# Kernel tuning notes

Measured on AMD Instinct MI355X. Metric: run time of the kernel, lower is better.

The kernel has to match this reference:

```python
import jax, jax.numpy as jnp
import numpy as np

H = 2        # num_heads
C = 128      # in_channels
K_ORDER = 4
BETA = 0.5


def _gcn_conv(x, row, col, deg_inv, n):
    # x: [N, H, C]; adj_t = D^{-1} A^T where A[row, col] = 1
    # (adj_t @ x)[c] = deg_inv[c] * sum_{e: col_e == c} x[row_e]
    msg = x[row]  # [E, H, C]
    agg = jax.ops.segment_sum(msg, col, num_segments=n)  # [N, H, C]
    return agg * deg_inv[:, None, None]


def _attn_conv(qs, ks, vs):
    # linear (kernelized) attention, non-block path
    n = qs.shape[0]
    kvs = jnp.einsum('lhm,lhd->hmd', ks, vs)            # [H, C, C]
    qkvs = jnp.einsum('nhm,hmd->nhd', qs, kvs)          # [N, H, C]
    vs_sum = vs.sum(axis=0)                             # [H, C]
    num = qkvs + vs_sum[None, :, :]
    ks_sum = ks.sum(axis=0)                             # [H, C]
    qks_sum = jnp.einsum('nhm,hm->nh', qs, ks_sum)[:, :, None]  # [N, H, 1]
    den = qks_sum + jnp.asarray(n, qs.dtype)
    return num / den


def setup_inputs() -> dict:
    key = jax.random.key(0)
    ks = jax.random.split(key, 8)
    N, E = 100000, 1600000
    x = jax.random.normal(ks[0], (N, C), jnp.float32)
    edge_index = jax.random.randint(ks[1], (2, E), 0, N, jnp.int64)
    s_in = 1.0 / np.sqrt(C)
    s_out = 1.0 / np.sqrt(H * C * (K_ORDER + 1))
    Wq_w = jax.random.normal(ks[2], (C, H * C), jnp.float32) * s_in
    Wq_b = jax.random.normal(ks[3], (H * C,), jnp.float32) * s_in
    Wk_w = jax.random.normal(ks[4], (C, H * C), jnp.float32) * s_in
    Wk_b = jax.random.normal(ks[5], (H * C,), jnp.float32) * s_in
    Wo_w = jax.random.normal(ks[6], (H * C * (K_ORDER + 1), C), jnp.float32) * s_out
    Wo_b = jax.random.normal(ks[7], (C,), jnp.float32) * s_out
    return {"x": x, "edge_index": edge_index, "Wq_w": Wq_w, "Wq_b": Wq_b,
            "Wk_w": Wk_w, "Wk_b": Wk_b, "Wo_w": Wo_w, "Wo_b": Wo_b}


def reference(x, edge_index, Wq_w, Wq_b, Wk_w, Wk_b, Wo_w, Wo_b):
    n = x.shape[0]
    row, col = edge_index[0], edge_index[1]
    # normalized adjacency D^{-1} A^T (pow(-1.0) in the source, not -0.5)
    deg = jax.ops.segment_sum(jnp.ones(row.shape[0], x.dtype), col, num_segments=n)
    deg_inv = jnp.where(deg > 0, 1.0 / deg, 0.0)

    query = (x @ Wq_w + Wq_b).reshape(n, H, C)
    key = (x @ Wk_w + Wk_b).reshape(n, H, C)
    qs = query / jnp.linalg.norm(query, axis=2, keepdims=True)
    ks = key / jnp.linalg.norm(key, axis=2, keepdims=True)

    x0 = jnp.broadcast_to(x[:, None, :], (n, H, C))  # [N, H, C]
    terms = [x0]
    for _ in range(K_ORDER):
        prev = terms[-1]
        gcn_i = _gcn_conv(prev, row, col, deg_inv, n)
        attn_i = _attn_conv(qs, ks, prev)
        terms.append(BETA * gcn_i + attn_i)
    xcat = jnp.concatenate(terms, axis=-1)  # [N, H, C*(K+1)]
    xcat = xcat.reshape(n, H * C * (K_ORDER + 1))
    return (xcat @ Wo_w + Wo_b) / H
```

## Files before the change

### kernel.cpp

```cpp
#include <hip/hip_runtime.h>

#define THREADS 256
#define NB 512
#define SEGCAP 6144
#define CSB 512

typedef __attribute__((ext_vector_type(8))) short short8;
typedef __attribute__((ext_vector_type(4))) float f32x4;

__device__ __forceinline__ float bf2f(unsigned short u) {
    union { unsigned int i; float f; } v;
    v.i = ((unsigned int)u) << 16;
    return v.f;
}
__device__ __forceinline__ unsigned short f2bf(float f) {
    union { float f; unsigned int i; } v;
    v.f = f;
    unsigned int r = (v.i + 0x7FFFu + ((v.i >> 16) & 1u)) >> 16;
    return (unsigned short)r;
}
__device__ __forceinline__ float4 ld4f(const float* p) {
    return *reinterpret_cast<const float4*>(p);
}
__device__ __forceinline__ float4 ld4f(const unsigned short* p) {
    ushort4 u = *reinterpret_cast<const ushort4*>(p);
    return make_float4(bf2f(u.x), bf2f(u.y), bf2f(u.z), bf2f(u.w));
}

__device__ __forceinline__ int edge_get(const int* base, int E, int mode, int which, int e) {
    size_t idx = (size_t)which * (size_t)E + (size_t)e;
    return mode ? base[2 * idx] : base[idx];
}

__global__ __launch_bounds__(256) void k_detect(const int* __restrict__ e, int E,
                                                int* __restrict__ mode) {
    __shared__ int nz;
    if (threadIdx.x == 0) nz = 0;
    __syncthreads();
    int lim = 2 * E;
    if (lim > 8192) lim = 8192;
    for (int i = 1 + 2 * (int)threadIdx.x; i < lim; i += 512)
        if (e[i] != 0) nz = 1;
    __syncthreads();
    if (threadIdx.x == 0) *mode = (nz == 0) ? 1 : 0;
}

__global__ __launch_bounds__(256) void k_hist(const int* __restrict__ eb, int E,
                                              const int* __restrict__ mode, int N, int CW, int epb,
                                              int* __restrict__ gcnt) {
    __shared__ int hist[NB];
    for (int i = threadIdx.x; i < NB; i += 256) hist[i] = 0;
    __syncthreads();
    int m = *mode;
    int e0 = blockIdx.x * epb;
    int e1 = min(e0 + epb, E);
    for (int e = e0 + threadIdx.x; e < e1; e += 256) {
        int c = edge_get(eb, E, m, 1, e);
        if ((unsigned)c < (unsigned)N) atomicAdd(&hist[c / CW], 1);
    }
    __syncthreads();
    for (int i = threadIdx.x; i < NB; i += 256)
        if (hist[i]) atomicAdd(&gcnt[i], hist[i]);
}

__global__ __launch_bounds__(NB) void k_bscan(const int* __restrict__ gcnt,
                                              int* __restrict__ gbase, int* __restrict__ gcursor) {
    __shared__ int s[NB];
    int t = threadIdx.x;
    int v = gcnt[t];
    s[t] = v;
    __syncthreads();
    for (int off = 1; off < NB; off <<= 1) {
        int add = (t >= off) ? s[t - off] : 0;
        __syncthreads();
        s[t] += add;
        __syncthreads();
    }
    gbase[t] = s[t] - v;
    gcursor[t] = s[t] - v;
}

__global__ __launch_bounds__(256) void k_part(const int* __restrict__ eb, int E,
                                              const int* __restrict__ mode, int N, int CW, int epb,
                                              int* __restrict__ gcursor, uint2* __restrict__ ebuf) {
    __shared__ int hist[NB];
    __shared__ int base[NB];
    for (int i = threadIdx.x; i < NB; i += 256) hist[i] = 0;
    __syncthreads();
    int m = *mode;
    int e0 = blockIdx.x * epb;
    int e1 = min(e0 + epb, E);
    for (int e = e0 + threadIdx.x; e < e1; e += 256) {
        int c = edge_get(eb, E, m, 1, e);
        if ((unsigned)c < (unsigned)N) atomicAdd(&hist[c / CW], 1);
    }
    __syncthreads();
    for (int i = threadIdx.x; i < NB; i += 256) {
        int h = hist[i];
        base[i] = h ? atomicAdd(&gcursor[i], h) : 0;
        hist[i] = 0;
    }
    __syncthreads();
    for (int e = e0 + threadIdx.x; e < e1; e += 256) {
        int c = edge_get(eb, E, m, 1, e);
        if ((unsigned)c < (unsigned)N) {
            int r = edge_get(eb, E, m, 0, e);
            if ((unsigned)r >= (unsigned)N) r = 0;
            int b = c / CW;
            int li = atomicAdd(&hist[b], 1);
            ebuf[(size_t)base[b] + li] = make_uint2((unsigned)r, (unsigned)c);
        }
    }
}

__global__ __launch_bounds__(256) void k_build(const uint2* __restrict__ ebuf,
                                               const int* __restrict__ gbase,
                                               const int* __restrict__ gcnt, int N, int CW,
                                               int* __restrict__ cnt, int* __restrict__ offs,
                                               float* __restrict__ deg_inv, int* __restrict__ csr) {
    __shared__ int hist[256];
    __shared__ int pfx[256];
    __shared__ int seg[SEGCAP];
    const int b = blockIdx.x;
    const int col0 = b * CW;
    const int ncols = min(CW, N - col0);
    if (ncols <= 0) return;
    const int ebase = gbase[b], ecnt = gcnt[b];
    const int t = threadIdx.x;
    for (int i = t; i < 256; i += 256) hist[i] = 0;
    __syncthreads();
    for (int e = t; e < ecnt; e += 256) {
        uint2 rc = ebuf[(size_t)ebase + e];
        atomicAdd(&hist[rc.y - col0], 1);
    }
    __syncthreads();
    int v = (t < ncols) ? hist[t] : 0;
    pfx[t] = v;
    __syncthreads();
    for (int off = 1; off < 256; off <<= 1) {
        int add = (t >= off) ? pfx[t - off] : 0;
        __syncthreads();
        pfx[t] += add;
        __syncthreads();
    }
    int excl = pfx[t] - v;
    if (t < ncols) {
        cnt[col0 + t] = v;
        offs[col0 + t] = ebase + excl;
        deg_inv[col0 + t] = (v > 0) ? 1.0f / (float)v : 0.0f;
    }
    __syncthreads();
    if (t < 256) hist[t] = (t < ncols) ? excl : 0;
    __syncthreads();
    if (ecnt <= SEGCAP) {
        for (int e = t; e < ecnt; e += 256) {
            uint2 rc = ebuf[(size_t)ebase + e];
            int li = atomicAdd(&hist[rc.y - col0], 1);
            seg[li] = (int)rc.x;
        }
        __syncthreads();
        for (int e = t; e < ecnt; e += 256) csr[(size_t)ebase + e] = seg[e];
    } else {
        for (int e = t; e < ecnt; e += 256) {
            uint2 rc = ebuf[(size_t)ebase + e];
            int li = atomicAdd(&hist[rc.y - col0], 1);
            csr[(size_t)ebase + li] = (int)rc.x;
        }
    }
}

__global__ __launch_bounds__(256) void k_prep_wqk(const float* __restrict__ Wq,
                                                  const float* __restrict__ Wk,
                                                  unsigned short* __restrict__ WqkT) {
    int i = blockIdx.x * 256 + threadIdx.x;
    if (i < 512 * 128) {
        int oc = i >> 7, k = i & 127;
        float v = (oc < 256) ? Wq[k * 256 + oc] : Wk[k * 256 + (oc - 256)];
        WqkT[i] = f2bf(v);
    }
}

__global__ __launch_bounds__(256) void k_prep_wo(const float* __restrict__ Wo,
                                                 unsigned short* __restrict__ WoT) {
    int i = blockIdx.x * 256 + threadIdx.x;
    if (i < 1280 * 128) {
        int r = i >> 7, j = i & 127;
        WoT[(size_t)j * 1280 + r] = f2bf(Wo[i]);
    }
}

__global__ __launch_bounds__(256) void k_prep_wo0(const float* __restrict__ Wo,
                                                  unsigned short* __restrict__ WoT0) {
    int i = blockIdx.x * 256 + threadIdx.x;
    if (i < 16384) {
        int j = i >> 7, c = i & 127;
        WoT0[i] = f2bf(Wo[(size_t)c * 128 + j] + Wo[(size_t)(640 + c) * 128 + j]);
    }
}

__global__ __launch_bounds__(256) void k_proj(const float* __restrict__ x,
                                              const unsigned short* __restrict__ WqkT,
                                              const float* __restrict__ bq,
                                              const float* __restrict__ bk,
                                              unsigned short* __restrict__ qs,
                                              unsigned short* __restrict__ ks, int N) {
    __shared__ unsigned short xs[64 * 128];
    __shared__ unsigned short os[64 * 256];
    const int t = threadIdx.x;
    const int n0 = blockIdx.x * 64;
#pragma unroll
    for (int i = 0; i < 4; i++) {
        int chunk = i * 256 + t;
        int r = chunk >> 4, c0 = (chunk & 15) * 8;
        float4 a0 = make_float4(0.f, 0.f, 0.f, 0.f), a1 = a0;
        if (n0 + r < N) {
            a0 = ld4f(&x[(size_t)(n0 + r) * 128 + c0]);
            a1 = ld4f(&x[(size_t)(n0 + r) * 128 + c0 + 4]);
        }
        short8 v = {(short)f2bf(a0.x), (short)f2bf(a0.y), (short)f2bf(a0.z), (short)f2bf(a0.w),
                    (short)f2bf(a1.x), (short)f2bf(a1.y), (short)f2bf(a1.z), (short)f2bf(a1.w)};
        int byte = r * 256 + ((c0 * 2) ^ ((r & 7) << 4));
        *reinterpret_cast<short8*>(reinterpret_cast<char*>(xs) + byte) = v;
    }
    __syncthreads();
    const int w = t >> 6, l = t & 63, lrow = l & 15, lhi = l >> 4;
    f32x4 acc[4][8];
    const f32x4 fz = {0.f, 0.f, 0.f, 0.f};
#pragma unroll
    for (int mt = 0; mt < 4; mt++)
#pragma unroll
        for (int nt = 0; nt < 8; nt++) acc[mt][nt] = fz;

    for (int kk = 0; kk < 4; kk++) {
        int kb = kk * 32 + lhi * 8;
        short8 af[4];
#pragma unroll
        for (int mt = 0; mt < 4; mt++) {
            int r = mt * 16 + lrow;
            af[mt] = *reinterpret_cast<const short8*>(
                reinterpret_cast<const char*>(xs) + r * 256 + ((kb * 2) ^ ((r & 7) << 4)));
        }
#pragma unroll
        for (int nt = 0; nt < 8; nt++) {
            int oc = w * 128 + nt * 16 + lrow;
            short8 bf = *reinterpret_cast<const short8*>(&WqkT[(size_t)oc * 128 + kb]);
#pragma unroll
            for (int mt = 0; mt < 4; mt++)
                acc[mt][nt] = __builtin_amdgcn_mfma_f32_16x16x32_bf16(af[mt], bf, acc[mt][nt], 0, 0, 0);
        }
    }
#pragma unroll
    for (int nt = 0; nt < 8; nt++) {
        int oc = w * 128 + nt * 16 + lrow;
        float b = (oc < 256) ? bq[oc] : bk[oc - 256];
#pragma unroll
        for (int mt = 0; mt < 4; mt++)
#pragma unroll
            for (int reg = 0; reg < 4; reg++) acc[mt][nt][reg] += b;
    }
    const int hc = (w & 1) * 128;
    float rv[4][4];
#pragma unroll
    for (int mt = 0; mt < 4; mt++) {
        float ss[4] = {0.f, 0.f, 0.f, 0.f};
#pragma unroll
        for (int nt = 0; nt < 8; nt++)
#pragma unroll
            for (int reg = 0; reg < 4; reg++) ss[reg] += acc[mt][nt][reg] * acc[mt][nt][reg];
#pragma unroll
        for (int m_ = 1; m_ < 16; m_ <<= 1)
#pragma unroll
            for (int reg = 0; reg < 4; reg++) ss[reg] += __shfl_xor(ss[reg], m_);
#pragma unroll
        for (int reg = 0; reg < 4; reg++) rv[mt][reg] = rsqrtf(ss[reg]);
    }
    for (int pass = 0; pass < 2; pass++) {
        if ((w >> 1) == pass) {
#pragma unroll
            for (int mt = 0; mt < 4; mt++)
#pragma unroll
                for (int reg = 0; reg < 4; reg++) {
                    int r = mt * 16 + lhi * 4 + reg;
#pragma unroll
                    for (int nt = 0; nt < 8; nt++)
                        os[r * 256 + hc + nt * 16 + lrow] = f2bf(acc[mt][nt][reg] * rv[mt][reg]);
                }
        }
        __syncthreads();
        unsigned short* dstg = pass ? ks : qs;
#pragma unroll
        for (int i = 0; i < 8; i++) {
            int chunk = i * 256 + t;
            int r = chunk >> 5, c = (chunk & 31) * 8;
            int n = n0 + r;
            if (n < N)
                *reinterpret_cast<short8*>(&dstg[(size_t)n * 256 + c]) =
                    *reinterpret_cast<const short8*>(&os[r * 256 + c]);
        }
        __syncthreads();
    }
}

__global__ __launch_bounds__(256) void k_colsum(const unsigned short* __restrict__ ks, int N,
                                                float* __restrict__ part) {
    __shared__ float red[8][256];
    const int t = threadIdx.x;
    const int rl = t >> 5;
    const int c0 = (t & 31) * 8;
    const int stride = (N + CSB - 1) / CSB;
    const int r0 = blockIdx.x * stride;
    const int rend = min(r0 + stride, N);
    float s[8] = {0.f, 0.f, 0.f, 0.f, 0.f, 0.f, 0.f, 0.f};
    int r = r0 + rl;
    for (; r + 24 < rend; r += 32) {
        short8 v0 = *reinterpret_cast<const short8*>(&ks[(size_t)(r + 0) * 256 + c0]);
        short8 v1 = *reinterpret_cast<const short8*>(&ks[(size_t)(r + 8) * 256 + c0]);
        short8 v2 = *reinterpret_cast<const short8*>(&ks[(size_t)(r + 16) * 256 + c0]);
        short8 v3 = *reinterpret_cast<const short8*>(&ks[(size_t)(r + 24) * 256 + c0]);
#pragma unroll
        for (int j = 0; j < 8; j++)
            s[j] += bf2f((unsigned short)v0[j]) + bf2f((unsigned short)v1[j]) +
                    bf2f((unsigned short)v2[j]) + bf2f((unsigned short)v3[j]);
    }
    for (; r < rend; r += 8) {
        short8 v = *reinterpret_cast<const short8*>(&ks[(size_t)r * 256 + c0]);
#pragma unroll
        for (int j = 0; j < 8; j++) s[j] += bf2f((unsigned short)v[j]);
    }
#pragma unroll
    for (int j = 0; j < 8; j++) red[rl][c0 + j] = s[j];
    __syncthreads();
    float tot = 0.f;
#pragma unroll
    for (int g = 0; g < 8; g++) tot += red[g][t];
    part[blockIdx.x * 256 + t] = tot;
}

__global__ __launch_bounds__(256) void k_colsum2(const float* __restrict__ part,
                                                 float* __restrict__ ks_sum) {
    const int t = threadIdx.x;
    float s0 = 0.f, s1 = 0.f, s2 = 0.f, s3 = 0.f;
    for (int b = 0; b < CSB; b += 4) {
        s0 += part[(b + 0) * 256 + t];
        s1 += part[(b + 1) * 256 + t];
        s2 += part[(b + 2) * 256 + t];
        s3 += part[(b + 3) * 256 + t];
    }
    ks_sum[t] = (s0 + s1) + (s2 + s3);
}

__global__ __launch_bounds__(256) void k_den(const unsigned short* __restrict__ qs,
                                             const float* __restrict__ ks_sum,
                                             float* __restrict__ den, int N) {
    int w = threadIdx.x >> 6, lane = threadIdx.x & 63;
    int n = blockIdx.x * 4 + w;
    if (n >= N) return;
    float4 q = ld4f(&qs[(size_t)n * 256 + lane * 4]);
    float4 kv = *reinterpret_cast<const float4*>(&ks_sum[lane * 4]);
    float s = q.x * kv.x + q.y * kv.y + q.z * kv.z + q.w * kv.w;
#pragma unroll
    for (int off = 1; off < 32; off <<= 1) s += __shfl_xor(s, off);
    if ((lane & 31) == 0) den[n * 2 + (lane >> 5)] = s + (float)N;
}

__device__ __forceinline__ short8 frag_ld(const unsigned short* tile, int kb, int col) {
    const char* b = reinterpret_cast<const char*>(tile);
    int cb = (col * 2) ^ (((kb >> 3) & 3) << 5);
    short8 r;
#pragma unroll
    for (int i = 0; i < 8; i++)
        r[i] = (short)*reinterpret_cast<const unsigned short*>(b + (kb + i) * 512 + cb);
    return r;
}

__global__ __launch_bounds__(256) void k_kvs2x(const unsigned short* __restrict__ ks,
                                               const float* __restrict__ vs,
                                               float* __restrict__ partial,
                                               float* __restrict__ pvsum, int rows_per, int N) {
    __shared__ unsigned short kt[32 * 256];
    __shared__ unsigned short vt[32 * 256];
    __shared__ float vred[8][256];
    const int t = threadIdx.x;
    const int w = t >> 6, l = t & 63, lrow = l & 15, lhi = l >> 4;
    const int h = w >> 1, mhalf = w & 1;
    const int r0 = blockIdx.x * rows_per;
    const int rend = min(r0 + rows_per, N);

    const f32x4 fz = {0.f, 0.f, 0.f, 0.f};
    f32x4 acc[4][8];
#pragma unroll
    for (int mt = 0; mt < 4; mt++)
#pragma unroll
        for (int nt = 0; nt < 8; nt++) acc[mt][nt] = fz;
    float vsum8[8] = {0.f, 0.f, 0.f, 0.f, 0.f, 0.f, 0.f, 0.f};

    for (int c0 = r0; c0 < rend; c0 += 32) {
#pragma unroll
        for (int i = 0; i < 4; i++) {
            int chunk = i * 256 + t;
            int n = chunk >> 5, cc = (chunk & 31) * 8;
            short8 v = {0, 0, 0, 0, 0, 0, 0, 0};
            if (c0 + n < rend)
                v = *reinterpret_cast<const short8*>(&ks[(size_t)(c0 + n) * 256 + cc]);
            *reinterpret_cast<short8*>(reinterpret_cast<char*>(kt) + n * 512 +
                                       ((cc * 2) ^ (((n >> 3) & 3) << 5))) = v;
        }
#pragma unroll
        for (int i = 0; i < 4; i++) {
            int chunk = i * 256 + t;
            int n = chunk >> 5, cc = (chunk & 31) * 8;
            float4 a0 = make_float4(0.f, 0.f, 0.f, 0.f), a1 = a0;
            if (c0 + n < rend) {
                a0 = ld4f(&vs[(size_t)(c0 + n) * 128 + (cc & 127)]);
                a1 = ld4f(&vs[(size_t)(c0 + n) * 128 + ((cc + 4) & 127)]);
            }
            unsigned short u0 = f2bf(a0.x), u1 = f2bf(a0.y), u2 = f2bf(a0.z), u3 = f2bf(a0.w);
            unsigned short u4 = f2bf(a1.x), u5 = f2bf(a1.y), u6 = f2bf(a1.z), u7 = f2bf(a1.w);
            vsum8[0] += bf2f(u0); vsum8[1] += bf2f(u1); vsum8[2] += bf2f(u2); vsum8[3] += bf2f(u3);
            vsum8[4] += bf2f(u4); vsum8[5] += bf2f(u5); vsum8[6] += bf2f(u6); vsum8[7] += bf2f(u7);
            short8 v = {(short)u0, (short)u1, (short)u2, (short)u3,
                        (short)u4, (short)u5, (short)u6, (short)u7};
            *reinterpret_cast<short8*>(reinterpret_cast<char*>(vt) + n * 512 +
                                       ((cc * 2) ^ (((n >> 3) & 3) << 5))) = v;
        }
        __syncthreads();
        {
            int kb = lhi * 8;
            short8 af[4];
#pragma unroll
            for (int mt = 0; mt < 4; mt++)
                af[mt] = frag_ld(vt, kb, h * 128 + mhalf * 64 + mt * 16 + lrow);
#pragma unroll
            for (int nt = 0; nt < 8; nt++) {
                short8 bf = frag_ld(kt, kb, h * 128 + nt * 16 + lrow);
#pragma unroll
                for (int mt = 0; mt < 4; mt++)
                    acc[mt][nt] =
                        __builtin_amdgcn_mfma_f32_16x16x32_bf16(af[mt], bf, acc[mt][nt], 0, 0, 0);
            }
        }
        __syncthreads();
    }
    float* pb = &partial[((size_t)blockIdx.x * 2 + h) * 16384];
#pragma unroll
    for (int mt = 0; mt < 4; mt++)
#pragma unroll
        for (int reg = 0; reg < 4; reg++) {
            int c_local = mhalf * 64 + mt * 16 + lhi * 4 + reg;
#pragma unroll
            for (int nt = 0; nt < 8; nt++) pb[c_local * 128 + nt * 16 + lrow] = acc[mt][nt][reg];
        }
    {
        int cc = (t & 31) * 8;
#pragma unroll
        for (int j = 0; j < 8; j++) vred[t >> 5][cc + j] = vsum8[j];
        __syncthreads();
        float s = 0.f;
#pragma unroll
        for (int r = 0; r < 8; r++) s += vred[r][t];
        pvsum[blockIdx.x * 256 + t] = s;
    }
}

__global__ __launch_bounds__(256) void k_kvsterm(const unsigned short* __restrict__ ks,
                                                 const unsigned short* __restrict__ qs,
                                                 const unsigned short* __restrict__ gbuf,
                                                 const unsigned short* __restrict__ kvsTp,
                                                 const float* __restrict__ vs_sum_p,
                                                 const float* __restrict__ den,
                                                 unsigned short* __restrict__ cur,
                                                 float* __restrict__ partial,
                                                 float* __restrict__ pvsum, int rows_per, int N) {
    __shared__ unsigned short kt[32 * 256];
    __shared__ unsigned short vt[32 * 256];
    __shared__ float vred[8][256];
    const int t = threadIdx.x;
    const int w = t >> 6, l = t & 63, lrow = l & 15, lhi = l >> 4;
    const int h = w >> 1, jh = w & 1;
    const int r0 = blockIdx.x * rows_per;
    const int rend = min(r0 + rows_per, N);

    const f32x4 fz = {0.f, 0.f, 0.f, 0.f};
    f32x4 acc[4][8];
#pragma unroll
    for (int mt = 0; mt < 4; mt++)
#pragma unroll
        for (int nt = 0; nt < 8; nt++) acc[mt][nt] = fz;
    float vsum8[8] = {0.f, 0.f, 0.f, 0.f, 0.f, 0.f, 0.f, 0.f};

    for (int c0 = r0; c0 < rend; c0 += 32) {
#pragma unroll
        for (int i = 0; i < 4; i++) {
            int chunk = i * 256 + t;
            int r = chunk >> 5, cc = (chunk & 31) * 8;
            int n = c0 + r;
            short8 g = {0, 0, 0, 0, 0, 0, 0, 0}, q = g;
            if (n < rend) {
                g = *reinterpret_cast<const short8*>(&gbuf[(size_t)n * 256 + cc]);
                q = *reinterpret_cast<const short8*>(&qs[(size_t)n * 256 + cc]);
            }
            int swz = (cc * 2) ^ ((r & 7) << 4);
            *reinterpret_cast<short8*>(reinterpret_cast<char*>(kt) + r * 512 + swz) = g;
            *reinterpret_cast<short8*>(reinterpret_cast<char*>(vt) + r * 512 + swz) = q;
        }
        __syncthreads();
        f32x4 acc2[2][4];
#pragma unroll
        for (int mt = 0; mt < 2; mt++)
#pragma unroll
            for (int nt = 0; nt < 4; nt++) acc2[mt][nt] = fz;
        for (int kk = 0; kk < 4; kk++) {
            int kb = kk * 32 + lhi * 8;
            short8 af[2];
#pragma unroll
            for (int mt = 0; mt < 2; mt++) {
                int r = mt * 16 + lrow;
                af[mt] = *reinterpret_cast<const short8*>(
                    reinterpret_cast<const char*>(vt) + r * 512 +
                    (((h * 128 + kb) * 2) ^ ((r & 7) << 4)));
            }
#pragma unroll
            for (int nt = 0; nt < 4; nt++) {
                int c = jh * 64 + nt * 16 + lrow;
                short8 bf =
                    *reinterpret_cast<const short8*>(&kvsTp[((size_t)h * 128 + c) * 128 + kb]);
#pragma unroll
                for (int mt = 0; mt < 2; mt++)
                    acc2[mt][nt] =
                        __builtin_amdgcn_mfma_f32_16x16x32_bf16(af[mt], bf, acc2[mt][nt], 0, 0, 0);
            }
        }
        __syncthreads();
#pragma unroll
        for (int mt = 0; mt < 2; mt++) {
#pragma unroll
            for (int reg = 0; reg < 4; reg++) {
                int r = mt * 16 + lhi * 4 + reg;
                int n = c0 + r;
                if (n < rend) {
                    float idn = 1.0f / den[n * 2 + h];
#pragma unroll
                    for (int nt = 0; nt < 4; nt++) {
                        int c = h * 128 + jh * 64 + nt * 16 + lrow;
                        float g = bf2f(*reinterpret_cast<const unsigned short*>(
                            reinterpret_cast<const char*>(kt) + r * 512 +
                            ((c * 2) ^ ((r & 7) << 4))));
                        float v = g + (acc2[mt][nt][reg] + vs_sum_p[c]) * idn;
                        *reinterpret_cast<unsigned short*>(reinterpret_cast<char*>(vt) + r * 512 +
                                                           ((c * 2) ^ (((r >> 3) & 3) << 5))) =
                            f2bf(v);
                    }
                } else {
#pragma unroll
                    for (int nt = 0; nt < 4; nt++) {
                        int c = h * 128 + jh * 64 + nt * 16 + lrow;
                        *reinterpret_cast<unsigned short*>(reinterpret_cast<char*>(vt) + r * 512 +
                                                           ((c * 2) ^ (((r >> 3) & 3) << 5))) = 0;
                    }
                }
            }
        }
        __syncthreads();
#pragma unroll
        for (int i = 0; i < 4; i++) {
            int chunk = i * 256 + t;
            int r = chunk >> 5, cc = (chunk & 31) * 8;
            int n = c0 + r;
            short8 v = *reinterpret_cast<const short8*>(
                reinterpret_cast<const char*>(vt) + r * 512 + ((cc * 2) ^ (((r >> 3) & 3) << 5)));
#pragma unroll
            for (int j = 0; j < 8; j++) vsum8[j] += bf2f((unsigned short)v[j]);
            if (n < rend) *reinterpret_cast<short8*>(&cur[(size_t)n * 256 + cc]) = v;
            short8 kv = {0, 0, 0, 0, 0, 0, 0, 0};
            if (n < rend) kv = *reinterpret_cast<const short8*>(&ks[(size_t)n * 256 + cc]);
            *reinterpret_cast<short8*>(reinterpret_cast<char*>(kt) + r * 512 +
                                       ((cc * 2) ^ (((r >> 3) & 3) << 5))) = kv;
        }
        __syncthreads();
        {
            int kb = lhi * 8;
            short8 af[4];
#pragma unroll
            for (int mt = 0; mt < 4; mt++)
                af[mt] = frag_ld(vt, kb, h * 128 + jh * 64 + mt * 16 + lrow);
#pragma unroll
            for (int nt = 0; nt < 8; nt++) {
                short8 bf = frag_ld(kt, kb, h * 128 + nt * 16 + lrow);
#pragma unroll
                for (int mt = 0; mt < 4; mt++)
                    acc[mt][nt] =
                        __builtin_amdgcn_mfma_f32_16x16x32_bf16(af[mt], bf, acc[mt][nt], 0, 0, 0);
            }
        }
        __syncthreads();
    }
    float* pb = &partial[((size_t)blockIdx.x * 2 + h) * 16384];
#pragma unroll
    for (int mt = 0; mt < 4; mt++)
#pragma unroll
        for (int reg = 0; reg < 4; reg++) {
            int c_local = jh * 64 + mt * 16 + lhi * 4 + reg;
#pragma unroll
            for (int nt = 0; nt < 8; nt++) pb[c_local * 128 + nt * 16 + lrow] = acc[mt][nt][reg];
        }
    {
        int cc = (t & 31) * 8;
#pragma unroll
        for (int j = 0; j < 8; j++) vred[t >> 5][cc + j] = vsum8[j];
        __syncthreads();
        float s = 0.f;
#pragma unroll
        for (int r = 0; r < 8; r++) s += vred[r][t];
        pvsum[blockIdx.x * 256 + t] = s;
    }
}

__global__ __launch_bounds__(256) void k_kvred(const float* __restrict__ partial,
                                               const float* __restrict__ pvsum, int S,
                                               unsigned short* __restrict__ kvsT,
                                               float* __restrict__ vs_sum) {
    if (blockIdx.x == 128) {
        int c = threadIdx.x;
        float s = 0.f;
        for (int i = 0; i < S; i++) s += pvsum[i * 256 + c];
        vs_sum[c] = s;
        return;
    }
    int e = blockIdx.x * 256 + threadIdx.x;
    float s0 = 0.f, s1 = 0.f, s2 = 0.f, s3 = 0.f, s4 = 0.f, s5 = 0.f, s6 = 0.f, s7 = 0.f;
    int i = 0;
    for (; i + 8 <= S; i += 8) {
        s0 += partial[(size_t)(i + 0) * 32768 + e];
        s1 += partial[(size_t)(i + 1) * 32768 + e];
        s2 += partial[(size_t)(i + 2) * 32768 + e];
        s3 += partial[(size_t)(i + 3) * 32768 + e];
        s4 += partial[(size_t)(i + 4) * 32768 + e];
        s5 += partial[(size_t)(i + 5) * 32768 + e];
        s6 += partial[(size_t)(i + 6) * 32768 + e];
        s7 += partial[(size_t)(i + 7) * 32768 + e];
    }
    for (; i < S; i++) s0 += partial[(size_t)i * 32768 + e];
    kvsT[e] = f2bf(((s0 + s1) + (s2 + s3)) + ((s4 + s5) + (s6 + s7)));
}

__global__ __launch_bounds__(256) void k_gather2(const unsigned short* __restrict__ prev,
                                                 const int* __restrict__ csr_src,
                                                 const int* __restrict__ offs,
                                                 const int* __restrict__ cnt,
                                                 const float* __restrict__ deg_inv,
                                                 unsigned short* __restrict__ cur, int N) {
    const int w = threadIdx.x >> 6, l = threadIdx.x & 63;
    int n = blockIdx.x * 4 + w;
    if (n >= N) return;
    const int start = offs[n], d = cnt[n];
    int e = start;
    const int eend = start + d;
    float a0 = 0.f, a1 = 0.f, a2 = 0.f, a3 = 0.f;
    const int co = l * 4;
    for (; e + 16 <= eend; e += 16) {
        int s[16];
#pragma unroll
        for (int i = 0; i < 16; i++) s[i] = csr_src[e + i];
        ushort4 u[16];
#pragma unroll
        for (int i = 0; i < 16; i++)
            u[i] = *reinterpret_cast<const ushort4*>(&prev[(size_t)s[i] * 256 + co]);
#pragma unroll
        for (int i = 0; i < 16; i++) {
            a0 += bf2f(u[i].x); a1 += bf2f(u[i].y); a2 += bf2f(u[i].z); a3 += bf2f(u[i].w);
        }
    }
    for (; e + 8 <= eend; e += 8) {
        int s[8];
#pragma unroll
        for (int i = 0; i < 8; i++) s[i] = csr_src[e + i];
        ushort4 u[8];
#pragma unroll
        for (int i = 0; i < 8; i++)
            u[i] = *reinterpret_cast<const ushort4*>(&prev[(size_t)s[i] * 256 + co]);
#pragma unroll
        for (int i = 0; i < 8; i++) {
            a0 += bf2f(u[i].x); a1 += bf2f(u[i].y); a2 += bf2f(u[i].z); a3 += bf2f(u[i].w);
        }
    }
    for (; e < eend; e++) {
        ushort4 u = *reinterpret_cast<const ushort4*>(&prev[(size_t)csr_src[e] * 256 + co]);
        a0 += bf2f(u.x); a1 += bf2f(u.y); a2 += bf2f(u.z); a3 += bf2f(u.w);
    }
    float sc = 0.5f * deg_inv[n];
    ushort4 o;
    o.x = f2bf(a0 * sc); o.y = f2bf(a1 * sc); o.z = f2bf(a2 * sc); o.w = f2bf(a3 * sc);
    *reinterpret_cast<ushort4*>(&cur[(size_t)n * 256 + co]) = o;
}

__global__ __launch_bounds__(256) void k_gather2f(const float* __restrict__ prev,
                                                  const int* __restrict__ csr_src,
                                                  const int* __restrict__ offs,
                                                  const int* __restrict__ cnt,
                                                  const float* __restrict__ deg_inv,
                                                  unsigned short* __restrict__ cur, int N) {
    const int w = threadIdx.x >> 6, l = threadIdx.x & 63;
    int n = blockIdx.x * 4 + w;
    if (n >= N) return;
    const int start = offs[n], d = cnt[n];
    int e = start;
    const int eend = start + d;
    float a0 = 0.f, a1 = 0.f;
    const int co = l * 2;
    for (; e + 16 <= eend; e += 16) {
        int s[16];
#pragma unroll
        for (int i = 0; i < 16; i++) s[i] = csr_src[e + i];
        float2 u[16];
#pragma unroll
        for (int i = 0; i < 16; i++)
            u[i] = *reinterpret_cast<const float2*>(&prev[(size_t)s[i] * 128 + co]);
#pragma unroll
        for (int i = 0; i < 16; i++) { a0 += u[i].x; a1 += u[i].y; }
    }
    for (; e + 8 <= eend; e += 8) {
        int s[8];
#pragma unroll
        for (int i = 0; i < 8; i++) s[i] = csr_src[e + i];
        float2 u[8];
#pragma unroll
        for (int i = 0; i < 8; i++)
            u[i] = *reinterpret_cast<const float2*>(&prev[(size_t)s[i] * 128 + co]);
#pragma unroll
        for (int i = 0; i < 8; i++) { a0 += u[i].x; a1 += u[i].y; }
    }
    for (; e < eend; e++) {
        float2 u = *reinterpret_cast<const float2*>(&prev[(size_t)csr_src[e] * 128 + co]);
        a0 += u.x; a1 += u.y;
    }
    float sc = 0.5f * deg_inv[n];
    ushort2 o;
    o.x = f2bf(a0 * sc); o.y = f2bf(a1 * sc);
    *reinterpret_cast<ushort2*>(&cur[(size_t)n * 256 + co]) = o;
    *reinterpret_cast<ushort2*>(&cur[(size_t)n * 256 + 128 + co]) = o;
}

template <int FIRST>
__global__ __launch_bounds__(256) void k_outflush(const float* __restrict__ x,
                                                  const unsigned short* __restrict__ ta,
                                                  const unsigned short* __restrict__ tb,
                                                  const unsigned short* __restrict__ WoT,
                                                  const unsigned short* __restrict__ WoT0,
                                                  const float* __restrict__ Wo_b,
                                                  float* __restrict__ out, int tblkA, int tblkB,
                                                  int N) {
    __shared__ unsigned short sm[64 * 256];
    const int t = threadIdx.x;
    const int n0 = blockIdx.x * 64;
    const int w = t >> 6, l = t & 63, lrow = l & 15, lhi = l >> 4;
    const f32x4 fz = {0.f, 0.f, 0.f, 0.f};
    f32x4 acc2[4][2];
#pragma unroll
    for (int mt = 0; mt < 4; mt++)
#pragma unroll
        for (int nt = 0; nt < 2; nt++) acc2[mt][nt] = fz;

    if (FIRST) {
#pragma unroll
        for (int i = 0; i < 4; i++) {
            int chunk = i * 256 + t;
            int r = chunk >> 4, c0 = (chunk & 15) * 8;
            float4 a0 = make_float4(0.f, 0.f, 0.f, 0.f), a1 = a0;
            if (n0 + r < N) {
                a0 = ld4f(&x[(size_t)(n0 + r) * 128 + c0]);
                a1 = ld4f(&x[(size_t)(n0 + r) * 128 + c0 + 4]);
            }
            short8 v = {(short)f2bf(a0.x), (short)f2bf(a0.y), (short)f2bf(a0.z), (short)f2bf(a0.w),
                        (short)f2bf(a1.x), (short)f2bf(a1.y), (short)f2bf(a1.z), (short)f2bf(a1.w)};
            *reinterpret_cast<short8*>(reinterpret_cast<char*>(sm) + r * 256 +
                                       ((c0 * 2) ^ ((r & 7) << 4))) = v;
        }
        __syncthreads();
        for (int kk = 0; kk < 4; kk++) {
            int kb = kk * 32 + lhi * 8;
            short8 af[4];
#pragma unroll
            for (int mt = 0; mt < 4; mt++) {
                int r = mt * 16 + lrow;
                af[mt] = *reinterpret_cast<const short8*>(
                    reinterpret_cast<const char*>(sm) + r * 256 + ((kb * 2) ^ ((r & 7) << 4)));
            }
#pragma unroll
            for (int nt = 0; nt < 2; nt++) {
                int j = w * 32 + nt * 16 + lrow;
                short8 bf = *reinterpret_cast<const short8*>(&WoT0[(size_t)j * 128 + kb]);
#pragma unroll
                for (int mt = 0; mt < 4; mt++)
                    acc2[mt][nt] =
                        __builtin_amdgcn_mfma_f32_16x16x32_bf16(af[mt], bf, acc2[mt][nt], 0, 0, 0);
            }
        }
        __syncthreads();
    }
#pragma unroll
    for (int b = 0; b < 2; b++) {
        const unsigned short* buf = b ? tb : ta;
        const int tblk = b ? tblkB : tblkA;
#pragma unroll
        for (int i = 0; i < 8; i++) {
            int chunk = i * 256 + t;
            int r = chunk >> 5, c0 = (chunk & 31) * 8;
            short8 v = {0, 0, 0, 0, 0, 0, 0, 0};
            if (n0 + r < N) v = *reinterpret_cast<const short8*>(&buf[(size_t)(n0 + r) * 256 + c0]);
            *reinterpret_cast<short8*>(reinterpret_cast<char*>(sm) + r * 512 +
                                       ((c0 * 2) ^ ((r & 7) << 4))) = v;
        }
        __syncthreads();
        for (int kk = 0; kk < 8; kk++) {
            int kb = kk * 32 + lhi * 8;
            short8 af[4];
#pragma unroll
            for (int mt = 0; mt < 4; mt++) {
                int r = mt * 16 + lrow;
                af[mt] = *reinterpret_cast<const short8*>(
                    reinterpret_cast<const char*>(sm) + r * 512 + ((kb * 2) ^ ((r & 7) << 4)));
            }
            int woff = (kb >> 7) * 640 + tblk * 128 + (kb & 127);
#pragma unroll
            for (int nt = 0; nt < 2; nt++) {
                int j = w * 32 + nt * 16 + lrow;
                short8 bf = *reinterpret_cast<const short8*>(&WoT[(size_t)j * 1280 + woff]);
#pragma unroll
                for (int mt = 0; mt < 4; mt++)
                    acc2[mt][nt] =
                        __builtin_amdgcn_mfma_f32_16x16x32_bf16(af[mt], bf, acc2[mt][nt], 0, 0, 0);
            }
        }
        __syncthreads();
    }
#pragma unroll
    for (int nt = 0; nt < 2; nt++) {
        int j = w * 32 + nt * 16 + lrow;
        float b = FIRST ? Wo_b[j] : 0.f;
#pragma unroll
        for (int mt = 0; mt < 4; mt++)
#pragma unroll
            for (int reg = 0; reg < 4; reg++) {
                int n = n0 + mt * 16 + lhi * 4 + reg;
                if (n < N) {
                    if (FIRST)
                        out[(size_t)n * 128 + j] = 0.5f * (acc2[mt][nt][reg] + b);
                    else
                        out[(size_t)n * 128 + j] += 0.5f * acc2[mt][nt][reg];
                }
            }
    }
}

__global__ __launch_bounds__(256) void k_outflush2(const unsigned short* __restrict__ qs,
                                                   const unsigned short* __restrict__ gbuf,
                                                   const unsigned short* __restrict__ kvsT,
                                                   const float* __restrict__ vs_sum,
                                                   const float* __restrict__ den,
                                                   const unsigned short* __restrict__ t3,
                                                   const unsigned short* __restrict__ WoT,
                                                   float* __restrict__ out, int N) {
    __shared__ unsigned short sm[64 * 256];
    const int t = threadIdx.x;
    const int n0 = blockIdx.x * 64;
    const int w = t >> 6, l = t & 63, lrow = l & 15, lhi = l >> 4;
    const f32x4 fz = {0.f, 0.f, 0.f, 0.f};

    short8 cv[8];
#pragma unroll
    for (int i = 0; i < 8; i++) {
        int chunk = i * 256 + t;
        int r = chunk >> 5, c0 = (chunk & 31) * 8;
        short8 v = {0, 0, 0, 0, 0, 0, 0, 0};
        if (n0 + r < N) v = *reinterpret_cast<const short8*>(&gbuf[(size_t)(n0 + r) * 256 + c0]);
        cv[i] = v;
    }
#pragma unroll
    for (int i = 0; i < 8; i++) {
        int chunk = i * 256 + t;
        int r = chunk >> 5, c0 = (chunk & 31) * 8;
        short8 v = {0, 0, 0, 0, 0, 0, 0, 0};
        if (n0 + r < N) v = *reinterpret_cast<const short8*>(&qs[(size_t)(n0 + r) * 256 + c0]);
        *reinterpret_cast<short8*>(reinterpret_cast<char*>(sm) + r * 512 +
                                   ((c0 * 2) ^ ((r & 7) << 4))) = v;
    }
    __syncthreads();
    const int h = w >> 1, jh = w & 1;
    f32x4 acc[4][4];
#pragma unroll
    for (int mt = 0; mt < 4; mt++)
#pragma unroll
        for (int nt = 0; nt < 4; nt++) acc[mt][nt] = fz;
    for (int kk = 0; kk < 4; kk++) {
        int kb = kk * 32 + lhi * 8;
        short8 af[4];
#pragma unroll
        for (int mt = 0; mt < 4; mt++) {
            int r = mt * 16 + lrow;
            af[mt] = *reinterpret_cast<const short8*>(
                reinterpret_cast<const char*>(sm) + r * 512 +
                (((h * 128 + kb) * 2) ^ ((r & 7) << 4)));
        }
#pragma unroll
        for (int nt = 0; nt < 4; nt++) {
            int c = jh * 64 + nt * 16 + lrow;
            short8 bf = *reinterpret_cast<const short8*>(&kvsT[((size_t)h * 128 + c) * 128 + kb]);
#pragma unroll
            for (int mt = 0; mt < 4; mt++)
                acc[mt][nt] = __builtin_amdgcn_mfma_f32_16x16x32_bf16(af[mt], bf, acc[mt][nt], 0, 0, 0);
        }
    }
    __syncthreads();
#pragma unroll
    for (int mt = 0; mt < 4; mt++) {
#pragma unroll
        for (int reg = 0; reg < 4; reg++) {
            int r = mt * 16 + lhi * 4 + reg;
            int n = n0 + r;
            if (n < N) {
                float idn = 1.0f / den[n * 2 + h];
#pragma unroll
                for (int nt = 0; nt < 4; nt++) {
                    int c = h * 128 + jh * 64 + nt * 16 + lrow;
                    *reinterpret_cast<unsigned short*>(reinterpret_cast<char*>(sm) + r * 512 +
                                                       ((c * 2) ^ ((r & 7) << 4))) =
                        f2bf((acc[mt][nt][reg] + vs_sum[c]) * idn);
                }
            }
        }
    }
    __syncthreads();
#pragma unroll
    for (int i = 0; i < 8; i++) {
        int chunk = i * 256 + t;
        int r = chunk >> 5, c0 = (chunk & 31) * 8;
        char* loc = reinterpret_cast<char*>(sm) + r * 512 + ((c0 * 2) ^ ((r & 7) << 4));
        short8 a = *reinterpret_cast<const short8*>(loc);
        short8 o;
#pragma unroll
        for (int j = 0; j < 8; j++)
            o[j] = (short)f2bf(bf2f((unsigned short)cv[i][j]) + bf2f((unsigned short)a[j]));
        *reinterpret_cast<short8*>(loc) = o;
    }
    __syncthreads();
    f32x4 acc2[4][2];
#pragma unroll
    for (int mt = 0; mt < 4; mt++)
#pragma unroll
        for (int nt = 0; nt < 2; nt++) acc2[mt][nt] = fz;
    for (int kk = 0; kk < 8; kk++) {
        int kb = kk * 32 + lhi * 8;
        short8 af[4];
#pragma unroll
        for (int mt = 0; mt < 4; mt++) {
            int r = mt * 16 + lrow;
            af[mt] = *reinterpret_cast<const short8*>(
                reinterpret_cast<const char*>(sm) + r * 512 + ((kb * 2) ^ ((r & 7) << 4)));
        }
        int woff = (kb >> 7) * 640 + 4 * 128 + (kb & 127);
#pragma unroll
        for (int nt = 0; nt < 2; nt++) {
            int j = w * 32 + nt * 16 + lrow;
            short8 bf = *reinterpret_cast<const short8*>(&WoT[(size_t)j * 1280 + woff]);
#pragma unroll
            for (int mt = 0; mt < 4; mt++)
                acc2[mt][nt] = __builtin_amdgcn_mfma_f32_16x16x32_bf16(af[mt], bf, acc2[mt][nt], 0, 0, 0);
        }
    }
    __syncthreads();
#pragma unroll
    for (int i = 0; i < 8; i++) {
        int chunk = i * 256 + t;
        int r = chunk >> 5, c0 = (chunk & 31) * 8;
        short8 v = {0, 0, 0, 0, 0, 0, 0, 0};
        if (n0 + r < N) v = *reinterpret_cast<const short8*>(&t3[(size_t)(n0 + r) * 256 + c0]);
        *reinterpret_cast<short8*>(reinterpret_cast<char*>(sm) + r * 512 +
                                   ((c0 * 2) ^ ((r & 7) << 4))) = v;
    }
    __syncthreads();
    for (int kk = 0; kk < 8; kk++) {
        int kb = kk * 32 + lhi * 8;
        short8 af[4];
#pragma unroll
        for (int mt = 0; mt < 4; mt++) {
            int r = mt * 16 + lrow;
            af[mt] = *reinterpret_cast<const short8*>(
                reinterpret_cast<const char*>(sm) + r * 512 + ((kb * 2) ^ ((r & 7) << 4)));
        }
        int woff = (kb >> 7) * 640 + 3 * 128 + (kb & 127);
#pragma unroll
        for (int nt = 0; nt < 2; nt++) {
            int j = w * 32 + nt * 16 + lrow;
            short8 bf = *reinterpret_cast<const short8*>(&WoT[(size_t)j * 1280 + woff]);
#pragma unroll
            for (int mt = 0; mt < 4; mt++)
                acc2[mt][nt] = __builtin_amdgcn_mfma_f32_16x16x32_bf16(af[mt], bf, acc2[mt][nt], 0, 0, 0);
        }
    }
#pragma unroll
    for (int nt = 0; nt < 2; nt++) {
        int j = w * 32 + nt * 16 + lrow;
#pragma unroll
        for (int mt = 0; mt < 4; mt++)
#pragma unroll
            for (int reg = 0; reg < 4; reg++) {
                int n = n0 + mt * 16 + lhi * 4 + reg;
                if (n < N) out[(size_t)n * 128 + j] += 0.5f * acc2[mt][nt][reg];
            }
    }
}

extern "C" void kernel_launch(void* const* d_in, const int* in_sizes, int n_in,
                              void* d_out, int out_size, void* d_ws, size_t ws_size,
                              hipStream_t stream) {
    const int N = in_sizes[0] / 128;
    const int E = in_sizes[1] / 2;
    const float* x = (const float*)d_in[0];
    const int* eraw = (const int*)d_in[1];
    const float* Wq_w = (const float*)d_in[2];
    const float* Wq_b = (const float*)d_in[3];
    const float* Wk_w = (const float*)d_in[4];
    const float* Wk_b = (const float*)d_in[5];
    const float* Wo_w = (const float*)d_in[6];
    const float* Wo_b = (const float*)d_in[7];
    float* out = (float*)d_out;

    char* p = (char*)d_ws;
    auto alloc = [&](size_t bytes) -> void* {
        void* r = (void*)p;
        p += (bytes + 255) & ~(size_t)255;
        return r;
    };
    unsigned short* qs = (unsigned short*)alloc((size_t)N * 256 * 2);
    unsigned short* ks = (unsigned short*)alloc((size_t)N * 256 * 2);
    unsigned short* B1 = (unsigned short*)alloc((size_t)N * 256 * 2);
    unsigned short* B2 = (unsigned short*)alloc((size_t)N * 256 * 2);
    float* deg_inv = (float*)alloc((size_t)N * 4);
    float* den = (float*)alloc((size_t)N * 2 * 4);
    float* ks_sum = (float*)alloc(256 * 4);
    float* vs_sum = (float*)alloc(256 * 4);
    float* colpart = (float*)alloc((size_t)CSB * 256 * 4);
    unsigned short* WqkT = (unsigned short*)alloc(512 * 128 * 2);
    unsigned short* WoT = (unsigned short*)alloc(1280 * 128 * 2);
    unsigned short* WoT0 = (unsigned short*)alloc(128 * 128 * 2);
    unsigned short* kvsTb = (unsigned short*)alloc(32768 * 2);
    int* cnt = (int*)alloc((size_t)N * 4);
    int* offs = (int*)alloc((size_t)N * 4);
    int* gcnt = (int*)alloc(NB * 4);
    int* gbase = (int*)alloc(NB * 4);
    int* gcursor = (int*)alloc(NB * 4);
    int* mode = (int*)alloc(256);
    int* csr = (int*)alloc((size_t)E * 4);

    size_t used = (size_t)(p - (char*)d_ws);
    size_t rem = (ws_size > used + (1 << 20)) ? ws_size - used - (1 << 20) : 0;
    int S = (int)(rem / (32768 * 4 + 1024));
    if (S > 256) S = 256;
    if (S < 8) S = 8;
    float* partial = (float*)alloc((size_t)S * 32768 * 4);
    float* pvsum = (float*)alloc((size_t)S * 256 * 4);
    uint2* ebuf;
    if ((size_t)S * 32768 * 4 >= (size_t)E * 8)
        ebuf = (uint2*)partial;
    else
        ebuf = (uint2*)alloc((size_t)E * 8);
    const int rows_per = (N + S - 1) / S;

    const int CW = (N + NB - 1) / NB;
    const int EBLK = 256;
    const int epb = (E + EBLK - 1) / EBLK;

    hipMemsetAsync(gcnt, 0, NB * 4, stream);

    k_detect<<<1, 256, 0, stream>>>(eraw, E, mode);
    k_hist<<<EBLK, 256, 0, stream>>>(eraw, E, mode, N, CW, epb, gcnt);
    k_bscan<<<1, NB, 0, stream>>>(gcnt, gbase, gcursor);
    k_part<<<EBLK, 256, 0, stream>>>(eraw, E, mode, N, CW, epb, gcursor, ebuf);
    k_build<<<NB, 256, 0, stream>>>(ebuf, gbase, gcnt, N, CW, cnt, offs, deg_inv, csr);

    k_prep_wqk<<<256, 256, 0, stream>>>(Wq_w, Wk_w, WqkT);
    k_prep_wo<<<640, 256, 0, stream>>>(Wo_w, WoT);
    k_prep_wo0<<<64, 256, 0, stream>>>(Wo_w, WoT0);

    const int nb64 = (N + 63) / 64;
    k_proj<<<nb64, 256, 0, stream>>>(x, WqkT, Wq_b, Wk_b, qs, ks, N);
    k_colsum<<<CSB, 256, 0, stream>>>(ks, N, colpart);
    k_colsum2<<<1, 256, 0, stream>>>(colpart, ks_sum);
    k_den<<<(N + 3) / 4, 256, 0, stream>>>(qs, ks_sum, den, N);

    const int gb4 = (N + 3) / 4;

    k_kvs2x<<<S, 256, 0, stream>>>(ks, x, partial, pvsum, rows_per, N);
    k_kvred<<<129, 256, 0, stream>>>(partial, pvsum, S, kvsTb, vs_sum);
    k_gather2f<<<gb4, 256, 0, stream>>>(x, csr, offs, cnt, deg_inv, B1, N);

    k_kvsterm<<<S, 256, 0, stream>>>(ks, qs, B1, kvsTb, vs_sum, den, B1, partial, pvsum,
                                     rows_per, N);
    k_kvred<<<129, 256, 0, stream>>>(partial, pvsum, S, kvsTb, vs_sum);
    k_gather2<<<gb4, 256, 0, stream>>>(B1, csr, offs, cnt, deg_inv, B2, N);

    k_kvsterm<<<S, 256, 0, stream>>>(ks, qs, B2, kvsTb, vs_sum, den, B2, partial, pvsum,
                                     rows_per, N);
    k_kvred<<<129, 256, 0, stream>>>(partial, pvsum, S, kvsTb, vs_sum);
    k_outflush<1><<<nb64, 256, 0, stream>>>(x, B1, B2, WoT, WoT0, Wo_b, out, 1, 2, N);
    k_gather2<<<gb4, 256, 0, stream>>>(B2, csr, offs, cnt, deg_inv, B1, N);

    k_kvsterm<<<S, 256, 0, stream>>>(ks, qs, B1, kvsTb, vs_sum, den, B1, partial, pvsum,
                                     rows_per, N);
    k_kvred<<<129, 256, 0, stream>>>(partial, pvsum, S, kvsTb, vs_sum);
    k_gather2<<<gb4, 256, 0, stream>>>(B1, csr, offs, cnt, deg_inv, B2, N);

    k_outflush2<<<nb64, 256, 0, stream>>>(qs, B2, kvsTb, vs_sum, den, B1, WoT, out, N);
}
```

Before: 1.560 ms.

## Store KV partial sums in bf16 and double the split count

The per-block kvs partial matrices written by the kvs kernels are now rounded to bf16 instead of stored as fp32, and the reduction kernel converts them back before summing. With half the bytes per partial, the split count S can now go up to 512 row slices, so more blocks run in the kvs kernels. This is meant to cut the write and read traffic of the partial buffer and raise parallelism. The cost is extra rounding error in every partial sum and a longer serial reduction loop over S.

```diff
diff --git a/kernel.cpp b/kernel.cpp
--- a/kernel.cpp
+++ b/kernel.cpp
@@ -375,7 +375,7 @@
 
 __global__ __launch_bounds__(256) void k_kvs2x(const unsigned short* __restrict__ ks,
                                                const float* __restrict__ vs,
-                                               float* __restrict__ partial,
+                                               unsigned short* __restrict__ partial,
                                                float* __restrict__ pvsum, int rows_per, int N) {
     __shared__ unsigned short kt[32 * 256];
     __shared__ unsigned short vt[32 * 256];
@@ -441,14 +441,15 @@
         }
         __syncthreads();
     }
-    float* pb = &partial[((size_t)blockIdx.x * 2 + h) * 16384];
+    unsigned short* pb = &partial[((size_t)blockIdx.x * 2 + h) * 16384];
 #pragma unroll
     for (int mt = 0; mt < 4; mt++)
 #pragma unroll
         for (int reg = 0; reg < 4; reg++) {
             int c_local = mhalf * 64 + mt * 16 + lhi * 4 + reg;
 #pragma unroll
-            for (int nt = 0; nt < 8; nt++) pb[c_local * 128 + nt * 16 + lrow] = acc[mt][nt][reg];
+            for (int nt = 0; nt < 8; nt++)
+                pb[c_local * 128 + nt * 16 + lrow] = f2bf(acc[mt][nt][reg]);
         }
     {
         int cc = (t & 31) * 8;
@@ -469,7 +470,7 @@
                                                  const float* __restrict__ vs_sum_p,
                                                  const float* __restrict__ den,
                                                  unsigned short* __restrict__ cur,
-                                                 float* __restrict__ partial,
+                                                 unsigned short* __restrict__ partial,
                                                  float* __restrict__ pvsum, int rows_per, int N) {
     __shared__ unsigned short kt[32 * 256];
     __shared__ unsigned short vt[32 * 256];
@@ -594,14 +595,15 @@
         }
         __syncthreads();
     }
-    float* pb = &partial[((size_t)blockIdx.x * 2 + h) * 16384];
+    unsigned short* pb = &partial[((size_t)blockIdx.x * 2 + h) * 16384];
 #pragma unroll
     for (int mt = 0; mt < 4; mt++)
 #pragma unroll
         for (int reg = 0; reg < 4; reg++) {
             int c_local = jh * 64 + mt * 16 + lhi * 4 + reg;
 #pragma unroll
-            for (int nt = 0; nt < 8; nt++) pb[c_local * 128 + nt * 16 + lrow] = acc[mt][nt][reg];
+            for (int nt = 0; nt < 8; nt++)
+                pb[c_local * 128 + nt * 16 + lrow] = f2bf(acc[mt][nt][reg]);
         }
     {
         int cc = (t & 31) * 8;
@@ -615,7 +617,7 @@
     }
 }
 
-__global__ __launch_bounds__(256) void k_kvred(const float* __restrict__ partial,
+__global__ __launch_bounds__(256) void k_kvred(const unsigned short* __restrict__ partial,
                                                const float* __restrict__ pvsum, int S,
                                                unsigned short* __restrict__ kvsT,
                                                float* __restrict__ vs_sum) {
@@ -630,16 +632,16 @@
     float s0 = 0.f, s1 = 0.f, s2 = 0.f, s3 = 0.f, s4 = 0.f, s5 = 0.f, s6 = 0.f, s7 = 0.f;
     int i = 0;
     for (; i + 8 <= S; i += 8) {
-        s0 += partial[(size_t)(i + 0) * 32768 + e];
-        s1 += partial[(size_t)(i + 1) * 32768 + e];
-        s2 += partial[(size_t)(i + 2) * 32768 + e];
-        s3 += partial[(size_t)(i + 3) * 32768 + e];
-        s4 += partial[(size_t)(i + 4) * 32768 + e];
-        s5 += partial[(size_t)(i + 5) * 32768 + e];
-        s6 += partial[(size_t)(i + 6) * 32768 + e];
-        s7 += partial[(size_t)(i + 7) * 32768 + e];
-    }
-    for (; i < S; i++) s0 += partial[(size_t)i * 32768 + e];
+        s0 += bf2f(partial[(size_t)(i + 0) * 32768 + e]);
+        s1 += bf2f(partial[(size_t)(i + 1) * 32768 + e]);
+        s2 += bf2f(partial[(size_t)(i + 2) * 32768 + e]);
+        s3 += bf2f(partial[(size_t)(i + 3) * 32768 + e]);
+        s4 += bf2f(partial[(size_t)(i + 4) * 32768 + e]);
+        s5 += bf2f(partial[(size_t)(i + 5) * 32768 + e]);
+        s6 += bf2f(partial[(size_t)(i + 6) * 32768 + e]);
+        s7 += bf2f(partial[(size_t)(i + 7) * 32768 + e]);
+    }
+    for (; i < S; i++) s0 += bf2f(partial[(size_t)i * 32768 + e]);
     kvsT[e] = f2bf(((s0 + s1) + (s2 + s3)) + ((s4 + s5) + (s6 + s7)));
 }
 
@@ -1054,13 +1056,13 @@
 
     size_t used = (size_t)(p - (char*)d_ws);
     size_t rem = (ws_size > used + (1 << 20)) ? ws_size - used - (1 << 20) : 0;
-    int S = (int)(rem / (32768 * 4 + 1024));
-    if (S > 256) S = 256;
+    int S = (int)(rem / (32768 * 2 + 1024));
+    if (S > 512) S = 512;
     if (S < 8) S = 8;
-    float* partial = (float*)alloc((size_t)S * 32768 * 4);
+    unsigned short* partial = (unsigned short*)alloc((size_t)S * 32768 * 2);
     float* pvsum = (float*)alloc((size_t)S * 256 * 4);
     uint2* ebuf;
-    if ((size_t)S * 32768 * 4 >= (size_t)E * 8)
+    if ((size_t)S * 32768 * 2 >= (size_t)E * 8)
         ebuf = (uint2*)partial;
     else
         ebuf = (uint2*)alloc((size_t)E * 8);
```

Result: slower. 1.796 ms (median of 3 runs) (+15.1%).
